# Optimization experiments

Hardware: AMD Instinct MI355X
Metric: run time of the kernel (lower is better)

Reference implementation:

```python
import jax, jax.numpy as jnp
import numpy as np

B, S, H, NH = 1, 4096, 1024, 16
DH = H // NH


def setup_inputs() -> dict:
    key = jax.random.key(0)
    ks = jax.random.split(key, 9)
    sc = 0.02
    return {
        "queries": jax.random.normal(ks[0], (B, S, H), jnp.float32),
        "keys": jax.random.normal(ks[1], (B, S, H), jnp.float32),
        "values": jax.random.normal(ks[2], (B, S, H), jnp.float32),
        "Wq_w": jax.random.normal(ks[3], (H, H), jnp.float32) * sc,
        "Wq_b": jax.random.normal(ks[4], (H,), jnp.float32) * sc,
        "Wk_w": jax.random.normal(ks[5], (H, H), jnp.float32) * sc,
        "Wk_b": jax.random.normal(ks[6], (H,), jnp.float32) * sc,
        "Wv_w": jax.random.normal(ks[7], (H, H), jnp.float32) * sc,
        "Wv_b": jax.random.normal(ks[8], (H,), jnp.float32) * sc,
    }


def _split_heads(x):
    # torch.chunk(x, NH, dim=-1) then stack(dim=1) == reshape + transpose
    b, s, h = x.shape
    return jnp.transpose(x.reshape(b, s, NH, DH), (0, 2, 1, 3))  # [B,NH,S,DH]


def reference(queries, keys, values, Wq_w, Wq_b, Wk_w, Wk_b, Wv_w, Wv_b):
    q = jax.nn.relu(queries @ Wq_w.T + Wq_b)
    k = jax.nn.relu(keys @ Wk_w.T + Wk_b)
    v = jax.nn.relu(values @ Wv_w.T + Wv_b)
    qh, kh, vh = _split_heads(q), _split_heads(k), _split_heads(v)
    score = jnp.einsum("bhsd,bhtd->bhst", qh, kh) / jnp.sqrt(jnp.float32(DH))
    attn = jax.nn.softmax(score, axis=-1)
    a = jnp.einsum("bhst,bhtd->bhsd", attn, vh)  # [B,NH,S,DH]
    # faithful to torch: permute(0,1,3,2) -> [B,NH,DH,S], then reshape to (B,S,H)
    a = jnp.transpose(a, (0, 1, 3, 2)).reshape(q.shape[0], q.shape[1], q.shape[2])
    return a + queries
```

## Files before the change

### kernel.cpp

```cpp
#include <hip/hip_runtime.h>
#include <stdint.h>


#define SEQ 4096
#define HID 1024
#define NHEAD 16
#define DHEAD 64

typedef __attribute__((ext_vector_type(8))) short short8_t;
typedef __attribute__((ext_vector_type(4))) float f32x4;
typedef __attribute__((ext_vector_type(16))) float f32x16;
typedef __attribute__((ext_vector_type(2))) unsigned int u32x2;

#define WS_WQ   12582912u
#define WS_QO   15728640u
#define WS_KO   19922944u
#define WS_VT   24117248u

__device__ __forceinline__ unsigned short f2bf(float f) {
  union { float f; unsigned int u; } x; x.f = f;
  unsigned int u = x.u;
  return (unsigned short)((u + 0x7FFFu + ((u >> 16) & 1u)) >> 16);
}

__device__ __forceinline__ float fexp2(float x) {
#if __has_builtin(__builtin_amdgcn_exp2f)
  return __builtin_amdgcn_exp2f(x);
#else
  float r; asm("v_exp_f32 %0, %1" : "=v"(r) : "v"(x)); return r;
#endif
}

__device__ __forceinline__ unsigned int pk2(float a, float b) {
  unsigned int r;
  asm("v_cvt_pk_bf16_f32 %0, %1, %2" : "=v"(r) : "v"(a), "v"(b));
  return r;
}

__device__ __forceinline__ void pl32swap(unsigned int& a, unsigned int& b) {
  asm("v_permlane32_swap_b32 %0, %1" : "+v"(a), "+v"(b));
}

__device__ __forceinline__ void gll16(const void* g, void* l) {
  __builtin_amdgcn_global_load_lds(
      (const __attribute__((address_space(1))) void*)g,
      (__attribute__((address_space(3))) void*)l, 16, 0, 0);
}

__device__ __forceinline__ void packP(const f32x16& a, short8_t& p0,
                                      short8_t& p1) {
  unsigned int w0 = pk2(a[0], a[1]),   w1 = pk2(a[2], a[3]);
  unsigned int w2 = pk2(a[4], a[5]),   w3 = pk2(a[6], a[7]);
  unsigned int w4 = pk2(a[8], a[9]),   w5 = pk2(a[10], a[11]);
  unsigned int w6 = pk2(a[12], a[13]), w7 = pk2(a[14], a[15]);
  pl32swap(w0, w2);
  pl32swap(w1, w3);
  pl32swap(w4, w6);
  pl32swap(w5, w7);
  union { unsigned int u[4]; short8_t v; } q0, q1;
  q0.u[0] = w0; q0.u[1] = w1; q0.u[2] = w2; q0.u[3] = w3;
  q1.u[0] = w4; q1.u[1] = w5; q1.u[2] = w6; q1.u[3] = w7;
  p0 = q0.v; p1 = q1.v;
}

#define MFMA32(a, b, c) __builtin_amdgcn_mfma_f32_32x32x16_bf16(a, b, c, 0, 0, 0)

__global__ void __launch_bounds__(256) prep_w(
    const float* __restrict__ wq, const float* __restrict__ wk,
    const float* __restrict__ wv, unsigned short* __restrict__ ws) {
  const int i = blockIdx.x * 256 + threadIdx.x;
  const int which = i >> 18;
  const int off = (i & 262143) << 2;
  const float* src = which == 0 ? wq : (which == 1 ? wk : wv);
  unsigned short* dst = ws + WS_WQ + (unsigned)which * 1048576u;
  float4 f = *(const float4*)(src + off);
  u32x2 p;
  p.x = pk2(f.x, f.y);
  p.y = pk2(f.z, f.w);
  *(u32x2*)(dst + off) = p;
}

__global__ void __launch_bounds__(256) qkv_gemm(
    unsigned short* __restrict__ ws, const float* __restrict__ qin,
    const float* __restrict__ kin, const float* __restrict__ vin,
    const float* __restrict__ bq, const float* __restrict__ bk,
    const float* __restrict__ bv) {
  __shared__ alignas(16) unsigned short lA[128 * 64];
  __shared__ alignas(16) unsigned short lB[128 * 64];
  const int z = blockIdx.z;
  const float* A32 = z == 0 ? qin : (z == 1 ? kin : vin);
  const unsigned short* W = ws + WS_WQ + z * 1048576u;
  const float* bias = z == 0 ? bq : (z == 1 ? bk : bv);
  const int tid = threadIdx.x;
  const int lane = tid & 63;
  const int wid = tid >> 6;
  const int wr = wid >> 1, wc = wid & 1;
  const int lin = blockIdx.y * 8 + blockIdx.x;
  const int nid = (lin & 7) * 32 + (lin >> 3);
  const int bm = nid >> 3, bn = nid & 7;
  const int l15 = lane & 15, l4 = lane >> 4;

  f32x4 acc[4][4];
#pragma unroll
  for (int m = 0; m < 4; ++m)
#pragma unroll
    for (int n = 0; n < 4; ++n) acc[m][n] = {0.f, 0.f, 0.f, 0.f};

  const int srow = tid >> 3;
  const int sch = tid & 7;

  float4 ar[4][2];
#define LOADA(kt_)                                                             \
  {                                                                            \
    _Pragma("unroll") for (int rr = 0; rr < 4; ++rr) {                         \
      const int row = rr * 32 + srow;                                          \
      const float* s_ = A32 + (size_t)(bm * 128 + row) * 1024 + (kt_) +        \
                        sch * 8;                                               \
      ar[rr][0] = *(const float4*)(s_);                                        \
      ar[rr][1] = *(const float4*)(s_ + 4);                                    \
    }                                                                          \
  }
#define WRITEA()                                                               \
  {                                                                            \
    _Pragma("unroll") for (int rr = 0; rr < 4; ++rr) {                         \
      const int row = rr * 32 + srow;                                          \
      union { unsigned int u[4]; short8_t v; } t_;                             \
      t_.u[0] = pk2(ar[rr][0].x, ar[rr][0].y);                                 \
      t_.u[1] = pk2(ar[rr][0].z, ar[rr][0].w);                                 \
      t_.u[2] = pk2(ar[rr][1].x, ar[rr][1].y);                                 \
      t_.u[3] = pk2(ar[rr][1].z, ar[rr][1].w);                                 \
      *(short8_t*)((char*)lA + row * 128 + (((sch ^ (row & 7))) * 16)) = t_.v; \
    }                                                                          \
  }

  LOADA(0);
  for (int kt = 0; kt < 1024; kt += 64) {
    __syncthreads();
    WRITEA();
#pragma unroll
    for (int r = 0; r < 4; ++r) {
      const int row = r * 32 + srow;
      const int ch = sch ^ (row & 7);
      gll16(W + (size_t)(bn * 128 + row) * 1024 + kt + ch * 8,
            (char*)lB + r * 4096 + wid * 1024);
    }
    __syncthreads();
    if (kt + 64 < 1024) LOADA(kt + 64);
    short8_t af[4][2], bf[4][2];
#pragma unroll
    for (int m = 0; m < 4; ++m) {
      const int row = wr * 64 + m * 16 + l15;
#pragma unroll
      for (int kk = 0; kk < 2; ++kk)
        af[m][kk] = *(const short8_t*)(
            (const char*)lA + row * 128 + (((kk * 4 + l4) ^ (row & 7)) * 16));
    }
#pragma unroll
    for (int n = 0; n < 4; ++n) {
      const int row = wc * 64 + n * 16 + l15;
#pragma unroll
      for (int kk = 0; kk < 2; ++kk)
        bf[n][kk] = *(const short8_t*)(
            (const char*)lB + row * 128 + (((kk * 4 + l4) ^ (row & 7)) * 16));
    }
#pragma unroll
    for (int m = 0; m < 4; ++m)
#pragma unroll
      for (int n = 0; n < 4; ++n)
#pragma unroll
        for (int kk = 0; kk < 2; ++kk)
          acc[m][n] = __builtin_amdgcn_mfma_f32_16x16x32_bf16(
              af[m][kk], bf[n][kk], acc[m][n], 0, 0, 0);
  }
#undef LOADA
#undef WRITEA

  const int row0 = bm * 128 + wr * 64;
  const int col0 = bn * 128 + wc * 64;
  if (z < 2) {
    const float scl = (z == 1) ? 0.18033688011112042f : 1.0f;
    unsigned short* o = ws + WS_QO + z * 4194304u;
#pragma unroll
    for (int n = 0; n < 4; ++n) {
      const int col = col0 + n * 16 + l15;
      const float bb = bias[col];
#pragma unroll
      for (int m = 0; m < 4; ++m)
#pragma unroll
        for (int j = 0; j < 4; ++j) {
          const int row = row0 + m * 16 + l4 * 4 + j;
          o[(size_t)row * 1024 + col] = f2bf(fmaxf(acc[m][n][j] + bb, 0.f) * scl);
        }
    }
  } else {
    unsigned short* vt = ws + WS_VT;
#pragma unroll
    for (int n = 0; n < 4; ++n) {
      const int col = col0 + n * 16 + l15;
      const float bb = bias[col];
      const int nh = col >> 6, d = col & 63;
#pragma unroll
      for (int m = 0; m < 4; ++m) {
        const int t0 = row0 + m * 16 + l4 * 4;
        u32x2 p;
        p.x = f2bf(fmaxf(acc[m][n][0] + bb, 0.f)) |
              ((unsigned int)f2bf(fmaxf(acc[m][n][1] + bb, 0.f)) << 16);
        p.y = f2bf(fmaxf(acc[m][n][2] + bb, 0.f)) |
              ((unsigned int)f2bf(fmaxf(acc[m][n][3] + bb, 0.f)) << 16);
        *(u32x2*)(vt + (size_t)nh * 262144 + (size_t)d * 4096 + t0) = p;
      }
    }
  }
}

__global__ void __launch_bounds__(512, 4) attn_fwd(
    const unsigned short* __restrict__ ws, const float* __restrict__ qin,
    float* __restrict__ out) {
  __shared__ alignas(16) char smem[32768];
  const char* lKb = smem;
  const char* lVb = smem + 16384;
  float* fO = (float*)smem;
  float* fRs = (float*)(smem + 16896);

  const unsigned short* qo = ws + WS_QO;
  const char* koB = (const char*)(ws + WS_KO);
  const char* vtB = (const char*)(ws + WS_VT);
  const int nh = blockIdx.y;
  const int qb0 = blockIdx.x * 128;
  const int tid = threadIdx.x, lane = tid & 63, wid = tid >> 6;
  const int l31 = lane & 31, l5 = lane >> 5;
  const int qg = wid >> 1, tw = wid & 1;
  const int sq = qb0 + qg * 32 + l31;

  const int stt = tid >> 3;
  const int sch = tid & 7;
  const unsigned kgoff =
      (unsigned)(stt * 1024 + nh * 64 + ((sch ^ (stt & 7)) * 8)) * 2u;
  const unsigned vgoff =
      (unsigned)(nh * 262144 + stt * 4096 + ((sch ^ (stt & 7)) * 8)) * 2u;
  const unsigned ldst = (unsigned)tid * 16u;

  short8_t qf[4];
#pragma unroll
  for (int kcd = 0; kcd < 4; ++kcd)
    qf[kcd] = *(const short8_t*)(qo + (size_t)sq * 1024 + nh * 64 +
                                 kcd * 16 + l5 * 8);

  int kofl[4];
  {
    const int row = tw * 32 + l31;
#pragma unroll
    for (int kcd = 0; kcd < 4; ++kcd)
      kofl[kcd] = row * 128 + (((kcd * 2 + l5) ^ (row & 7)) * 16);
  }
  int vofl[2][2];
#pragma unroll
  for (int n = 0; n < 2; ++n) {
    const int row = n * 32 + l31;
#pragma unroll
    for (int kc = 0; kc < 2; ++kc)
      vofl[n][kc] = row * 128 + (((tw * 4 + kc * 2 + l5) ^ (row & 7)) * 16);
  }

  f32x16 zro;
#pragma unroll
  for (int r = 0; r < 16; ++r) zro[r] = 0.f;
  f32x16 aco0 = zro, aco1 = zro;
  float rs0 = 0.f, rs1 = 0.f, rs2 = 0.f, rs3 = 0.f;

#define STAGE(buf, kvb)                                                        \
  {                                                                            \
    gll16(koB + (kgoff + (unsigned)(kvb) * 2048u),                             \
          (char*)lKb + (buf) * 8192 + ldst);                                   \
    gll16(vtB + (vgoff + (unsigned)(kvb) * 2u),                                \
          (char*)lVb + (buf) * 8192 + ldst);                                   \
  }

  STAGE(0, 0);
  __syncthreads();
  int cur = 0;

  for (int kv = 0; kv < 4096; kv += 64) {
    if (kv + 64 < 4096) STAGE(cur ^ 1, kv + 64);
    const char* lKc = lKb + cur * 8192;
    const char* lVc = lVb + cur * 8192;

    __builtin_amdgcn_s_setprio(1);
    f32x16 acs = MFMA32(*(const short8_t*)(lKc + kofl[0]), qf[0], zro);
#pragma unroll
    for (int kcd = 1; kcd < 4; ++kcd)
      acs = MFMA32(*(const short8_t*)(lKc + kofl[kcd]), qf[kcd], acs);
    __builtin_amdgcn_s_setprio(0);

#pragma unroll
    for (int r = 0; r < 16; r += 4) {
      const float p0 = fexp2(acs[r]);
      const float p1 = fexp2(acs[r + 1]);
      const float p2 = fexp2(acs[r + 2]);
      const float p3 = fexp2(acs[r + 3]);
      acs[r] = p0; acs[r + 1] = p1; acs[r + 2] = p2; acs[r + 3] = p3;
      rs0 += p0; rs1 += p1; rs2 += p2; rs3 += p3;
    }

    short8_t pa0, pa1;
    packP(acs, pa0, pa1);

    const short8_t vf00 = *(const short8_t*)(lVc + vofl[0][0]);
    const short8_t vf10 = *(const short8_t*)(lVc + vofl[1][0]);
    const short8_t vf01 = *(const short8_t*)(lVc + vofl[0][1]);
    const short8_t vf11 = *(const short8_t*)(lVc + vofl[1][1]);
    __builtin_amdgcn_s_setprio(1);
    aco0 = MFMA32(pa0, vf00, aco0);
    aco1 = MFMA32(pa0, vf10, aco1);
    aco0 = MFMA32(pa1, vf01, aco0);
    aco1 = MFMA32(pa1, vf11, aco1);
    __builtin_amdgcn_s_setprio(0);

    __syncthreads();
    cur ^= 1;
  }

  float rs = (rs0 + rs1) + (rs2 + rs3);
  rs += __shfl_xor(rs, 32);

#pragma unroll 1
  for (int p = 0; p < 4; ++p) {
    if (qg == p) {
      float* myO = fO + tw * 2112;
#pragma unroll
      for (int r = 0; r < 16; ++r) {
        const int sl = (r & 3) + 8 * (r >> 2) + 4 * l5;
        myO[l31 * 33 + sl] = aco0[r];
        myO[(l31 + 32) * 33 + sl] = aco1[r];
      }
      if (l5 == 0) fRs[tw * 32 + l31] = rs;
    }
    __syncthreads();
    {
      const int s = tid & 31;
      const int dg = tid >> 5;
      const int sg = qb0 + p * 32 + s;
      const float inv = 1.f / (fRs[s] + fRs[32 + s]);
      const int scol = sg & 1023, srow = sg >> 10;
#pragma unroll
      for (int i = 0; i < 4; ++i) {
        const int d = dg * 4 + i;
        const float v = fO[d * 33 + s] + fO[2112 + d * 33 + s];
        const int idx = (nh * 256 + d * 4 + srow) * 1024 + scol;
        out[idx] = qin[idx] + v * inv;
      }
    }
    __syncthreads();
  }
#undef STAGE
}

extern "C" void kernel_launch(void* const* d_in, const int* in_sizes, int n_in,
                              void* d_out, int out_size, void* d_ws,
                              size_t ws_size, hipStream_t stream) {
  const float* qin = (const float*)d_in[0];
  const float* kin = (const float*)d_in[1];
  const float* vin = (const float*)d_in[2];
  const float* wq = (const float*)d_in[3];
  const float* bq = (const float*)d_in[4];
  const float* wk = (const float*)d_in[5];
  const float* bk = (const float*)d_in[6];
  const float* wv = (const float*)d_in[7];
  const float* bv = (const float*)d_in[8];
  unsigned short* ws = (unsigned short*)d_ws;
  float* out = (float*)d_out;

  prep_w<<<dim3(3072), dim3(256), 0, stream>>>(wq, wk, wv, ws);
  qkv_gemm<<<dim3(8, 32, 3), dim3(256), 0, stream>>>(ws, qin, kin, vin,
                                                     bq, bk, bv);
  attn_fwd<<<dim3(32, 16), dim3(512), 0, stream>>>(ws, qin, out);
}
```

Before: 130.9 us.

## Split attention over two KV halves with larger Q tiles and separate normalize kernel

The attention kernel now gives each block 256 queries instead of 128, so each K/V tile loaded into shared memory is reused by twice as many queries. It also splits the KV sequence into two halves across blockIdx.z, which keeps the grid at 512 blocks. Each half writes unnormalized bf16 partial outputs and per-row exp sums to the workspace, and a new elementwise kernel combines the halves, divides by the sums and adds the residual. The goal is to halve K/V shared-memory traffic per query. The cost is an extra launch, an extra round trip through global memory, and bf16 rounding of the partial sums.

```diff
diff --git a/kernel.cpp b/kernel.cpp
--- a/kernel.cpp
+++ b/kernel.cpp
@@ -21,6 +21,12 @@
   union { float f; unsigned int u; } x; x.f = f;
   unsigned int u = x.u;
   return (unsigned short)((u + 0x7FFFu + ((u >> 16) & 1u)) >> 16);
+}
+
+__device__ __forceinline__ float b2f(unsigned short h) {
+  union { unsigned int u; float f; } x;
+  x.u = (unsigned int)h << 16;
+  return x.f;
 }
 
 __device__ __forceinline__ float fexp2(float x) {
@@ -214,37 +220,41 @@
 }
 
 __global__ void __launch_bounds__(512, 4) attn_fwd(
-    const unsigned short* __restrict__ ws, const float* __restrict__ qin,
-    float* __restrict__ out) {
-  __shared__ alignas(16) char smem[32768];
-  const char* lKb = smem;
-  const char* lVb = smem + 16384;
+    unsigned short* __restrict__ ws) {
+  __shared__ alignas(16) char smem[35328];
   float* fO = (float*)smem;
-  float* fRs = (float*)(smem + 16896);
+  float* fRsL = (float*)(smem + 33280);
 
   const unsigned short* qo = ws + WS_QO;
   const char* koB = (const char*)(ws + WS_KO);
   const char* vtB = (const char*)(ws + WS_VT);
+  unsigned short* op = ws;
+  float* rsg = (float*)(ws + 8388608u);
   const int nh = blockIdx.y;
-  const int qb0 = blockIdx.x * 128;
+  const int kvh = blockIdx.z;
+  const int qb0 = blockIdx.x * 256;
   const int tid = threadIdx.x, lane = tid & 63, wid = tid >> 6;
   const int l31 = lane & 31, l5 = lane >> 5;
   const int qg = wid >> 1, tw = wid & 1;
-  const int sq = qb0 + qg * 32 + l31;
 
   const int stt = tid >> 3;
   const int sch = tid & 7;
   const unsigned kgoff =
-      (unsigned)(stt * 1024 + nh * 64 + ((sch ^ (stt & 7)) * 8)) * 2u;
+      (unsigned)(stt * 1024 + nh * 64 + ((sch ^ (stt & 7)) * 8)) * 2u +
+      (unsigned)kvh * 4194304u;
   const unsigned vgoff =
-      (unsigned)(nh * 262144 + stt * 4096 + ((sch ^ (stt & 7)) * 8)) * 2u;
+      (unsigned)(nh * 262144 + stt * 4096 + ((sch ^ (stt & 7)) * 8)) * 2u +
+      (unsigned)kvh * 4096u;
   const unsigned ldst = (unsigned)tid * 16u;
 
-  short8_t qf[4];
-#pragma unroll
-  for (int kcd = 0; kcd < 4; ++kcd)
-    qf[kcd] = *(const short8_t*)(qo + (size_t)sq * 1024 + nh * 64 +
-                                 kcd * 16 + l5 * 8);
+  short8_t qf[2][4];
+#pragma unroll
+  for (int c = 0; c < 2; ++c)
+#pragma unroll
+    for (int kcd = 0; kcd < 4; ++kcd)
+      qf[c][kcd] = *(const short8_t*)(
+          qo + (size_t)(qb0 + qg * 64 + c * 32 + l31) * 1024 + nh * 64 +
+          kcd * 16 + l5 * 8);
 
   int kofl[4];
   {
@@ -265,94 +275,149 @@
   f32x16 zro;
 #pragma unroll
   for (int r = 0; r < 16; ++r) zro[r] = 0.f;
-  f32x16 aco0 = zro, aco1 = zro;
-  float rs0 = 0.f, rs1 = 0.f, rs2 = 0.f, rs3 = 0.f;
-
-#define STAGE(buf, kvb)                                                        \
+  f32x16 aco00 = zro, aco01 = zro, aco10 = zro, aco11 = zro;
+  float rsa0 = 0.f, rsa1 = 0.f, rsa2 = 0.f, rsa3 = 0.f;
+  float rsb0 = 0.f, rsb1 = 0.f, rsb2 = 0.f, rsb3 = 0.f;
+
+#define STAGE(buf, ti)                                                         \
   {                                                                            \
-    gll16(koB + (kgoff + (unsigned)(kvb) * 2048u),                             \
-          (char*)lKb + (buf) * 8192 + ldst);                                   \
-    gll16(vtB + (vgoff + (unsigned)(kvb) * 2u),                                \
-          (char*)lVb + (buf) * 8192 + ldst);                                   \
+    gll16(koB + (kgoff + (unsigned)(ti) * 131072u),                            \
+          smem + (buf) * 16384 + ldst);                                        \
+    gll16(vtB + (vgoff + (unsigned)(ti) * 128u),                               \
+          smem + (buf) * 16384 + 8192 + ldst);                                 \
   }
 
   STAGE(0, 0);
   __syncthreads();
   int cur = 0;
 
-  for (int kv = 0; kv < 4096; kv += 64) {
-    if (kv + 64 < 4096) STAGE(cur ^ 1, kv + 64);
-    const char* lKc = lKb + cur * 8192;
-    const char* lVc = lVb + cur * 8192;
+  for (int i = 0; i < 32; ++i) {
+    if (i + 1 < 32) STAGE(cur ^ 1, i + 1);
+    const char* sK = smem + cur * 16384;
+    const char* sV = sK + 8192;
+
+    short8_t kfr[4];
+#pragma unroll
+    for (int kcd = 0; kcd < 4; ++kcd)
+      kfr[kcd] = *(const short8_t*)(sK + kofl[kcd]);
 
     __builtin_amdgcn_s_setprio(1);
-    f32x16 acs = MFMA32(*(const short8_t*)(lKc + kofl[0]), qf[0], zro);
-#pragma unroll
-    for (int kcd = 1; kcd < 4; ++kcd)
-      acs = MFMA32(*(const short8_t*)(lKc + kofl[kcd]), qf[kcd], acs);
+    f32x16 acs0 = MFMA32(kfr[0], qf[0][0], zro);
+    f32x16 acs1 = MFMA32(kfr[0], qf[1][0], zro);
+#pragma unroll
+    for (int kcd = 1; kcd < 4; ++kcd) {
+      acs0 = MFMA32(kfr[kcd], qf[0][kcd], acs0);
+      acs1 = MFMA32(kfr[kcd], qf[1][kcd], acs1);
+    }
     __builtin_amdgcn_s_setprio(0);
 
 #pragma unroll
     for (int r = 0; r < 16; r += 4) {
-      const float p0 = fexp2(acs[r]);
-      const float p1 = fexp2(acs[r + 1]);
-      const float p2 = fexp2(acs[r + 2]);
-      const float p3 = fexp2(acs[r + 3]);
-      acs[r] = p0; acs[r + 1] = p1; acs[r + 2] = p2; acs[r + 3] = p3;
-      rs0 += p0; rs1 += p1; rs2 += p2; rs3 += p3;
-    }
-
-    short8_t pa0, pa1;
-    packP(acs, pa0, pa1);
-
-    const short8_t vf00 = *(const short8_t*)(lVc + vofl[0][0]);
-    const short8_t vf10 = *(const short8_t*)(lVc + vofl[1][0]);
-    const short8_t vf01 = *(const short8_t*)(lVc + vofl[0][1]);
-    const short8_t vf11 = *(const short8_t*)(lVc + vofl[1][1]);
+      const float a0 = fexp2(acs0[r]),     a1 = fexp2(acs0[r + 1]);
+      const float a2 = fexp2(acs0[r + 2]), a3 = fexp2(acs0[r + 3]);
+      acs0[r] = a0; acs0[r + 1] = a1; acs0[r + 2] = a2; acs0[r + 3] = a3;
+      rsa0 += a0; rsa1 += a1; rsa2 += a2; rsa3 += a3;
+      const float b0 = fexp2(acs1[r]),     b1 = fexp2(acs1[r + 1]);
+      const float b2 = fexp2(acs1[r + 2]), b3 = fexp2(acs1[r + 3]);
+      acs1[r] = b0; acs1[r + 1] = b1; acs1[r + 2] = b2; acs1[r + 3] = b3;
+      rsb0 += b0; rsb1 += b1; rsb2 += b2; rsb3 += b3;
+    }
+
+    short8_t pa00, pa01, pa10, pa11;
+    packP(acs0, pa00, pa01);
+    packP(acs1, pa10, pa11);
+
+    const short8_t vf00 = *(const short8_t*)(sV + vofl[0][0]);
+    const short8_t vf10 = *(const short8_t*)(sV + vofl[1][0]);
+    const short8_t vf01 = *(const short8_t*)(sV + vofl[0][1]);
+    const short8_t vf11 = *(const short8_t*)(sV + vofl[1][1]);
+
     __builtin_amdgcn_s_setprio(1);
-    aco0 = MFMA32(pa0, vf00, aco0);
-    aco1 = MFMA32(pa0, vf10, aco1);
-    aco0 = MFMA32(pa1, vf01, aco0);
-    aco1 = MFMA32(pa1, vf11, aco1);
+    aco00 = MFMA32(pa00, vf00, aco00);
+    aco10 = MFMA32(pa10, vf00, aco10);
+    aco01 = MFMA32(pa00, vf10, aco01);
+    aco11 = MFMA32(pa10, vf10, aco11);
+    aco00 = MFMA32(pa01, vf01, aco00);
+    aco10 = MFMA32(pa11, vf01, aco10);
+    aco01 = MFMA32(pa01, vf11, aco01);
+    aco11 = MFMA32(pa11, vf11, aco11);
     __builtin_amdgcn_s_setprio(0);
 
     __syncthreads();
     cur ^= 1;
   }
-
-  float rs = (rs0 + rs1) + (rs2 + rs3);
-  rs += __shfl_xor(rs, 32);
-
+#undef STAGE
+
+  float rsA = (rsa0 + rsa1) + (rsa2 + rsa3);
+  float rsB = (rsb0 + rsb1) + (rsb2 + rsb3);
+  rsA += __shfl_xor(rsA, 32);
+  rsB += __shfl_xor(rsB, 32);
+  if (l5 == 0) {
+    fRsL[tw * 256 + qg * 64 + l31] = rsA;
+    fRsL[tw * 256 + qg * 64 + 32 + l31] = rsB;
+  }
+  __syncthreads();
+  if (tid < 256)
+    rsg[(kvh * 16 + nh) * 4096 + qb0 + tid] = fRsL[tid] + fRsL[256 + tid];
+
+  const unsigned onb = (unsigned)(kvh * 16 + nh) * 262144u;
 #pragma unroll 1
   for (int p = 0; p < 4; ++p) {
     if (qg == p) {
-      float* myO = fO + tw * 2112;
+      float* myO = fO + tw * 4160;
 #pragma unroll
       for (int r = 0; r < 16; ++r) {
         const int sl = (r & 3) + 8 * (r >> 2) + 4 * l5;
-        myO[l31 * 33 + sl] = aco0[r];
-        myO[(l31 + 32) * 33 + sl] = aco1[r];
+        myO[l31 * 65 + sl] = aco00[r];
+        myO[(l31 + 32) * 65 + sl] = aco01[r];
+        myO[l31 * 65 + 32 + sl] = aco10[r];
+        myO[(l31 + 32) * 65 + 32 + sl] = aco11[r];
       }
-      if (l5 == 0) fRs[tw * 32 + l31] = rs;
     }
     __syncthreads();
     {
-      const int s = tid & 31;
-      const int dg = tid >> 5;
-      const int sg = qb0 + p * 32 + s;
-      const float inv = 1.f / (fRs[s] + fRs[32 + s]);
-      const int scol = sg & 1023, srow = sg >> 10;
-#pragma unroll
-      for (int i = 0; i < 4; ++i) {
-        const int d = dg * 4 + i;
-        const float v = fO[d * 33 + s] + fO[2112 + d * 33 + s];
-        const int idx = (nh * 256 + d * 4 + srow) * 1024 + scol;
-        out[idx] = qin[idx] + v * inv;
+      const int s = tid & 63;
+      const int dg = tid >> 6;
+      const unsigned ob = onb + (unsigned)(qb0 + p * 64 + s);
+#pragma unroll
+      for (int j = 0; j < 8; ++j) {
+        const int d = dg * 8 + j;
+        const float v = fO[d * 65 + s] + fO[4160 + d * 65 + s];
+        op[ob + (unsigned)d * 4096u] = f2bf(v);
       }
     }
     __syncthreads();
   }
-#undef STAGE
+}
+
+__global__ void __launch_bounds__(256) attn_norm(
+    const unsigned short* __restrict__ ws, const float* __restrict__ qin,
+    float* __restrict__ out) {
+  const int e = blockIdx.x * 256 + threadIdx.x;
+  const int qq = e & 1023;
+  const int nd = e >> 10;
+  const int nh = nd >> 6, d = nd & 63;
+  const int q0 = qq * 4;
+  const unsigned short* op = ws;
+  const float* rsg = (const float*)(ws + 8388608u);
+  const unsigned ob = (unsigned)nd * 4096u + (unsigned)q0;
+  const u32x2 a = *(const u32x2*)(op + ob);
+  const u32x2 b = *(const u32x2*)(op + 4194304u + ob);
+  const float4 r0 = *(const float4*)(rsg + nh * 4096 + q0);
+  const float4 r1 = *(const float4*)(rsg + 65536 + nh * 4096 + q0);
+  const int srow = q0 >> 10, scol = q0 & 1023;
+  const int idx = (nh * 256 + d * 4 + srow) * 1024 + scol;
+  const float4 qv = *(const float4*)(qin + idx);
+  float4 o;
+  o.x = (b2f((unsigned short)(a.x & 0xffff)) +
+         b2f((unsigned short)(b.x & 0xffff))) / (r0.x + r1.x) + qv.x;
+  o.y = (b2f((unsigned short)(a.x >> 16)) +
+         b2f((unsigned short)(b.x >> 16))) / (r0.y + r1.y) + qv.y;
+  o.z = (b2f((unsigned short)(a.y & 0xffff)) +
+         b2f((unsigned short)(b.y & 0xffff))) / (r0.z + r1.z) + qv.z;
+  o.w = (b2f((unsigned short)(a.y >> 16)) +
+         b2f((unsigned short)(b.y >> 16))) / (r0.w + r1.w) + qv.w;
+  *(float4*)(out + idx) = o;
 }
 
 extern "C" void kernel_launch(void* const* d_in, const int* in_sizes, int n_in,
@@ -373,5 +438,6 @@
   prep_w<<<dim3(3072), dim3(256), 0, stream>>>(wq, wk, wv, ws);
   qkv_gemm<<<dim3(8, 32, 3), dim3(256), 0, stream>>>(ws, qin, kin, vin,
                                                      bq, bk, bv);
-  attn_fwd<<<dim3(32, 16), dim3(512), 0, stream>>>(ws, qin, out);
-}
+  attn_fwd<<<dim3(16, 16, 2), dim3(512), 0, stream>>>(ws);
+  attn_norm<<<dim3(4096), dim3(256), 0, stream>>>(ws, qin, out);
+}
```

Result: slower. 253.6 us (+93.7%).
